# Kernel tuning notes

Hardware: AMD Instinct MI355X
Metric: run time of the kernel (lower is better)

The kernel has to match this reference:

```python
import jax, jax.numpy as jnp
import numpy as np

B, S, D, H, DH = 2, 2048, 1024, 16, 64


def setup_inputs() -> dict:
    key = jax.random.key(0)
    ks = jax.random.split(key, 8)
    std = 0.02
    Q = jax.random.normal(ks[0], (B, S, D), jnp.float32)
    K = jax.random.normal(ks[1], (B, S, D), jnp.float32)
    V = jax.random.normal(ks[2], (B, S, D), jnp.float32)
    # 0/1 float mask, 1 = masked out (causal upper triangle), shape [B, S, S]
    causal = jnp.triu(jnp.ones((S, S), jnp.float32), k=1)
    attn_mask = jnp.broadcast_to(causal, (B, S, S))
    Wq = jax.random.normal(ks[3], (D, H * DH), jnp.float32) * std
    Wk = jax.random.normal(ks[4], (D, H * DH), jnp.float32) * std
    Wv = jax.random.normal(ks[5], (D, H * DH), jnp.float32) * std
    Wo = jax.random.normal(ks[6], (H * DH, D), jnp.float32) * std
    bq = jnp.zeros((H * DH,), jnp.float32)
    bk = jnp.zeros((H * DH,), jnp.float32)
    bv = jnp.zeros((H * DH,), jnp.float32)
    bo = jnp.zeros((D,), jnp.float32)
    return dict(Q=Q, K=K, V=V, attn_mask=attn_mask,
                Wq=Wq, bq=bq, Wk=Wk, bk=bk, Wv=Wv, bv=bv, Wo=Wo, bo=bo)


def reference(Q, K, V, attn_mask, Wq, bq, Wk, bk, Wv, bv, Wo, bo):
    b = Q.shape[0]
    # projections + split heads: [B, S, H*DH] -> [B, H, S, DH]
    def heads(x, W, bias):
        y = x @ W + bias
        return y.reshape(b, -1, H, DH).transpose(0, 2, 1, 3)
    Qh = heads(Q, Wq, bq)
    Kh = heads(K, Wk, bk)
    Vh = heads(V, Wv, bv)
    scale = jnp.sqrt(jnp.asarray(DH, jnp.float32))
    # [B, H, Sq, Sk]
    scores = jnp.einsum('bhqd,bhkd->bhqk', Qh, Kh) / scale
    scores = scores - 1e9 * attn_mask[:, None, :, :]
    probs = jax.nn.softmax(scores, axis=-1)
    out = jnp.einsum('bhqk,bhkd->bhqd', probs, Vh)  # [B, H, Sq, DH]
    out = out.transpose(0, 2, 1, 3).reshape(b, -1, H * DH)
    return out @ Wo + bo
```

## Files before the change

### kernel.cpp

```cpp
#include <hip/hip_runtime.h>
#include <hip/hip_bf16.h>

#define S_LEN 2048
#define NH 16
#define DHD 64

typedef __attribute__((ext_vector_type(8))) short bf16x8;
typedef __attribute__((ext_vector_type(4))) float f32x4;

__device__ __forceinline__ f32x4 mfma16(bf16x8 a, bf16x8 b, f32x4 c) {
  return __builtin_amdgcn_mfma_f32_16x16x32_bf16(a, b, c, 0, 0, 0);
}

union Pack8 { int4 v; __hip_bfloat16 h[8]; };

__device__ __forceinline__ unsigned pack_bf16(float lo, float hi) {
  union { __hip_bfloat16 b; unsigned short s; } a0, a1;
  a0.b = __float2bfloat16(lo);
  a1.b = __float2bfloat16(hi);
  return (unsigned)a0.s | ((unsigned)a1.s << 16);
}

__global__ __launch_bounds__(256) void transpose_cast(
    const float* __restrict__ W0, const float* __restrict__ W1,
    const float* __restrict__ W2, const float* __restrict__ W3,
    __hip_bfloat16* __restrict__ T0, __hip_bfloat16* __restrict__ T1,
    __hip_bfloat16* __restrict__ T2, __hip_bfloat16* __restrict__ T3) {
  __shared__ float t[32][33];
  const float* W;
  __hip_bfloat16* T;
  switch (blockIdx.z) {
    case 0: W = W0; T = T0; break;
    case 1: W = W1; T = T1; break;
    case 2: W = W2; T = T2; break;
    default: W = W3; T = T3; break;
  }
  const int tx = threadIdx.x, ty = threadIdx.y;
  const int c = blockIdx.x * 32 + tx;
  const int r0 = blockIdx.y * 32;
#pragma unroll
  for (int i = ty; i < 32; i += 8) t[i][tx] = W[(r0 + i) * 1024 + c];
  __syncthreads();
  const int c0 = blockIdx.x * 32;
#pragma unroll
  for (int i = ty; i < 32; i += 8)
    T[(c0 + i) * 1024 + (r0 + tx)] = __float2bfloat16(t[tx][i]);
}

#define LDP 72

__global__ __launch_bounds__(256) void qkv_gemm(
    const float* __restrict__ Qx, const float* __restrict__ Kx,
    const float* __restrict__ Vx,
    const __hip_bfloat16* __restrict__ WqT, const __hip_bfloat16* __restrict__ WkT,
    const __hip_bfloat16* __restrict__ WvT,
    const float* __restrict__ bq, const float* __restrict__ bk,
    const float* __restrict__ bv,
    __hip_bfloat16* __restrict__ Qh, __hip_bfloat16* __restrict__ Kh,
    __hip_bfloat16* __restrict__ Vt) {
  __shared__ __hip_bfloat16 sA[128 * LDP];
  __shared__ __hip_bfloat16 sB[128 * LDP];
  const int K = 1024;
  const int yy = blockIdx.y;
  const int sel = yy >> 3;
  const int m0 = blockIdx.x * 128;
  const int n0 = (yy & 7) * 128;
  const float* X = sel == 0 ? Qx : sel == 1 ? Kx : Vx;
  const __hip_bfloat16* Bt = sel == 0 ? WqT : sel == 1 ? WkT : WvT;
  const float* bias = sel == 0 ? bq : sel == 1 ? bk : bv;
  __hip_bfloat16* outp = sel == 0 ? Qh : sel == 1 ? Kh : Vt;
  const float scale = sel == 0 ? 0.18033688011112042f : 1.0f;
  const int tid = threadIdx.x;
  const int lane = tid & 63;
  const int wv = tid >> 6;
  const int wm = (wv >> 1) * 64;
  const int wn = (wv & 1) * 64;
  const int rq = lane & 15;
  const int kg = lane >> 4;
  f32x4 acc[4][4] = {};
  for (int k0 = 0; k0 < K; k0 += 64) {
#pragma unroll
    for (int j = 0; j < 4; ++j) {
      const int cid = j * 256 + tid;
      const int row = cid >> 3;
      const int kc = (cid & 7) * 8;
      const float* ap = X + (m0 + row) * K + k0 + kc;
      float4 f0 = *(const float4*)ap;
      float4 f1 = *(const float4*)(ap + 4);
      Pack8 p;
      p.h[0] = __float2bfloat16(f0.x); p.h[1] = __float2bfloat16(f0.y);
      p.h[2] = __float2bfloat16(f0.z); p.h[3] = __float2bfloat16(f0.w);
      p.h[4] = __float2bfloat16(f1.x); p.h[5] = __float2bfloat16(f1.y);
      p.h[6] = __float2bfloat16(f1.z); p.h[7] = __float2bfloat16(f1.w);
      *(int4*)&sA[row * LDP + kc] = p.v;
      *(int4*)&sB[row * LDP + kc] = *(const int4*)(Bt + (n0 + row) * K + k0 + kc);
    }
    __syncthreads();
#pragma unroll
    for (int kk = 0; kk < 2; ++kk) {
      bf16x8 af[4], bfr[4];
      const int kcol = kk * 32 + kg * 8;
#pragma unroll
      for (int mi = 0; mi < 4; ++mi)
        af[mi] = *(const bf16x8*)&sA[(wm + mi * 16 + rq) * LDP + kcol];
#pragma unroll
      for (int ni = 0; ni < 4; ++ni)
        bfr[ni] = *(const bf16x8*)&sB[(wn + ni * 16 + rq) * LDP + kcol];
#pragma unroll
      for (int mi = 0; mi < 4; ++mi)
#pragma unroll
        for (int ni = 0; ni < 4; ++ni)
          acc[mi][ni] = mfma16(af[mi], bfr[ni], acc[mi][ni]);
    }
    __syncthreads();
  }
  const int cr = (lane >> 4) << 2;
  const int cc = lane & 15;
#pragma unroll
  for (int ni = 0; ni < 4; ++ni) {
    const int col = n0 + wn + ni * 16 + cc;
    const float bv_ = bias[col];
#pragma unroll
    for (int mi = 0; mi < 4; ++mi) {
      const int rowb = m0 + wm + mi * 16 + cr;
#pragma unroll
      for (int r = 0; r < 4; ++r) {
        const int row = rowb + r;
        const float v = (acc[mi][ni][r] + bv_) * scale;
        const int b = row >> 11, s = row & 2047, h = col >> 6, dh = col & 63;
        const __hip_bfloat16 hv = __float2bfloat16(v);
        if (sel < 2)
          outp[((b * NH + h) * S_LEN + s) * DHD + dh] = hv;
        else
          outp[((b * NH + h) * DHD + dh) * S_LEN + s] = hv;
      }
    }
  }
}

__global__ __launch_bounds__(256) void out_gemm(
    const __hip_bfloat16* __restrict__ Aptr, const __hip_bfloat16* __restrict__ Bt,
    const float* __restrict__ bias, float* __restrict__ outp) {
  __shared__ __hip_bfloat16 sA[128 * LDP];
  __shared__ __hip_bfloat16 sB[128 * LDP];
  const int K = 1024;
  const int m0 = blockIdx.x * 128;
  const int n0 = blockIdx.y * 128;
  const int tid = threadIdx.x;
  const int lane = tid & 63;
  const int wv = tid >> 6;
  const int wm = (wv >> 1) * 64;
  const int wn = (wv & 1) * 64;
  const int rq = lane & 15;
  const int kg = lane >> 4;
  f32x4 acc[4][4] = {};
  for (int k0 = 0; k0 < K; k0 += 64) {
#pragma unroll
    for (int j = 0; j < 4; ++j) {
      const int cid = j * 256 + tid;
      const int row = cid >> 3;
      const int kc = (cid & 7) * 8;
      *(int4*)&sA[row * LDP + kc] = *(const int4*)(Aptr + (m0 + row) * K + k0 + kc);
      *(int4*)&sB[row * LDP + kc] = *(const int4*)(Bt + (n0 + row) * K + k0 + kc);
    }
    __syncthreads();
#pragma unroll
    for (int kk = 0; kk < 2; ++kk) {
      bf16x8 af[4], bfr[4];
      const int kcol = kk * 32 + kg * 8;
#pragma unroll
      for (int mi = 0; mi < 4; ++mi)
        af[mi] = *(const bf16x8*)&sA[(wm + mi * 16 + rq) * LDP + kcol];
#pragma unroll
      for (int ni = 0; ni < 4; ++ni)
        bfr[ni] = *(const bf16x8*)&sB[(wn + ni * 16 + rq) * LDP + kcol];
#pragma unroll
      for (int mi = 0; mi < 4; ++mi)
#pragma unroll
        for (int ni = 0; ni < 4; ++ni)
          acc[mi][ni] = mfma16(af[mi], bfr[ni], acc[mi][ni]);
    }
    __syncthreads();
  }
  const int cr = (lane >> 4) << 2;
  const int cc = lane & 15;
#pragma unroll
  for (int ni = 0; ni < 4; ++ni) {
    const int col = n0 + wn + ni * 16 + cc;
    const float bv = bias[col];
#pragma unroll
    for (int mi = 0; mi < 4; ++mi) {
      const int rowb = m0 + wm + mi * 16 + cr;
#pragma unroll
      for (int r = 0; r < 4; ++r)
        outp[(rowb + r) * 1024 + col] = acc[mi][ni][r] + bv;
    }
  }
}

#define SLOT 2304
#define NSLOT 320

__global__ __launch_bounds__(256) void attn_fwd(
    const __hip_bfloat16* __restrict__ Qh, const __hip_bfloat16* __restrict__ Kh,
    const __hip_bfloat16* __restrict__ Vt, __hip_bfloat16* __restrict__ AttO,
    unsigned char* __restrict__ Part) {
  __shared__ __hip_bfloat16 sK[64 * 72];
  __shared__ __hip_bfloat16 sV[64 * 72];
  const int tid = threadIdx.x;
  const int lane = tid & 63;
  const int wv = tid >> 6;
  const int h = blockIdx.y, b = blockIdx.z;
  const int bh = b * NH + h;
  const int u = 79 - (int)blockIdx.x;
  int j, s;
  if (u < 8)       { j = u; s = 0; }
  else if (u < 24) { int v = u - 8;  j = 8 + (v >> 1);  s = v & 1; }
  else if (u < 48) { int v = u - 24; int q3 = v / 3; j = 16 + q3; s = v - 3 * q3; }
  else             { int v = u - 48; j = 24 + (v >> 2); s = v & 3; }
  const int ns = (j >> 3) + 1;
  const int kv_beg = s * 512;
  const int kv_end = min(kv_beg + 512, j * 64 + 64);
  const int nt = (kv_end - kv_beg + 63) >> 6;

  const int i_tile = 4 * j + wv;
  const int q0 = i_tile * 16;
  const int qmax = q0 + 15;
  const __hip_bfloat16* Qb = Qh + bh * (S_LEN * DHD);
  const __hip_bfloat16* Kb = Kh + bh * (S_LEN * DHD);
  const __hip_bfloat16* Vb = Vt + bh * (DHD * S_LEN);
  const int c = lane & 15;
  const int g = lane >> 4;
  const bf16x8 qf0 = *(const bf16x8*)&Qb[(q0 + c) * DHD + g * 8];
  const bf16x8 qf1 = *(const bf16x8*)&Qb[(q0 + c) * DHD + 32 + g * 8];
  f32x4 o[4] = {};
  float m_run = -1e30f, l_run = 0.f;
  const int idx_lo = c + ((lane & 16) << 1);
  const int idx_hi = idx_lo + 16;
  const int lim0 = q0 + c - (g << 2);
  const bool hi_half = (lane & 32) != 0;

  const int srow = tid >> 2;
  const int scol = (tid & 3) << 4;
  int4 ka0, ka1, va0, va1;
#define ISSUE_LOADS(KV0)                                                  \
  ka0 = *(const int4*)&Kb[(KV0 + srow) * DHD + scol];                     \
  ka1 = *(const int4*)&Kb[(KV0 + srow) * DHD + scol + 8];                 \
  va0 = *(const int4*)&Vb[srow * S_LEN + (KV0) + scol];                   \
  va1 = *(const int4*)&Vb[srow * S_LEN + (KV0) + scol + 8];
#define STORE_LDS()                                                       \
  *(int4*)&sK[srow * 72 + scol] = ka0;                                    \
  *(int4*)&sK[srow * 72 + scol + 8] = ka1;                                \
  *(int4*)&sV[srow * 72 + scol] = va0;                                    \
  *(int4*)&sV[srow * 72 + scol + 8] = va1;

  ISSUE_LOADS(kv_beg);
  STORE_LDS();
  __syncthreads();

  for (int t = 0; t < nt; ++t) {
    const int kv0 = kv_beg + t * 64;
    const bool havenext = (t + 1 < nt);
    if (havenext) { ISSUE_LOADS(kv0 + 64); }
    if (kv0 <= qmax) {
      f32x4 sc[4] = {};
#pragma unroll
      for (int fi = 0; fi < 4; ++fi) {
        const bf16x8 ka = *(const bf16x8*)&sK[(fi * 16 + c) * 72 + g * 8];
        const bf16x8 kb = *(const bf16x8*)&sK[(fi * 16 + c) * 72 + 32 + g * 8];
        sc[fi] = mfma16(ka, qf0, sc[fi]);
        sc[fi] = mfma16(kb, qf1, sc[fi]);
      }
      if (kv0 + 63 > q0) {
        const int lim = lim0 - kv0;
#pragma unroll
        for (int fi = 0; fi < 4; ++fi)
#pragma unroll
          for (int r = 0; r < 4; ++r)
            if (fi * 16 + r > lim) sc[fi][r] = -1e30f;
      }
      float pm = fmaxf(fmaxf(fmaxf(sc[0][0], sc[0][1]), fmaxf(sc[0][2], sc[0][3])),
                       fmaxf(fmaxf(sc[1][0], sc[1][1]), fmaxf(sc[1][2], sc[1][3])));
      pm = fmaxf(pm, fmaxf(fmaxf(fmaxf(sc[2][0], sc[2][1]), fmaxf(sc[2][2], sc[2][3])),
                           fmaxf(fmaxf(sc[3][0], sc[3][1]), fmaxf(sc[3][2], sc[3][3]))));
      pm = fmaxf(pm, __shfl_xor(pm, 16));
      pm = fmaxf(pm, __shfl_xor(pm, 32));
      if (__any(pm > m_run + 8.0f)) {
        const float mn = fmaxf(m_run, pm);
        const float al = __builtin_amdgcn_exp2f(m_run - mn);
        m_run = mn;
        l_run *= al;
#pragma unroll
        for (int jj = 0; jj < 4; ++jj)
#pragma unroll
          for (int r = 0; r < 4; ++r) o[jj][r] *= al;
      }
      f32x4 p[4];
      float ps = 0.f;
#pragma unroll
      for (int fi = 0; fi < 4; ++fi) {
#pragma unroll
        for (int r = 0; r < 4; ++r) {
          p[fi][r] = __builtin_amdgcn_exp2f(sc[fi][r] - m_run);
          ps += p[fi][r];
        }
      }
      ps += __shfl_xor(ps, 16);
      ps += __shfl_xor(ps, 32);
      l_run += ps;
      unsigned w0[4], w1[4];
#pragma unroll
      for (int fi = 0; fi < 4; ++fi) {
        w0[fi] = pack_bf16(p[fi][0], p[fi][1]);
        w1[fi] = pack_bf16(p[fi][2], p[fi][3]);
      }
#pragma unroll
      for (int kk = 0; kk < 2; ++kk) {
        const int fA = 2 * kk, fB = 2 * kk + 1;
        union { unsigned w[4]; bf16x8 v; } pa;
        unsigned a0 = __shfl((int)w0[fA], idx_lo), b0 = __shfl((int)w0[fB], idx_lo);
        unsigned a1 = __shfl((int)w1[fA], idx_lo), b1 = __shfl((int)w1[fB], idx_lo);
        unsigned a2 = __shfl((int)w0[fA], idx_hi), b2 = __shfl((int)w0[fB], idx_hi);
        unsigned a3 = __shfl((int)w1[fA], idx_hi), b3 = __shfl((int)w1[fB], idx_hi);
        pa.w[0] = hi_half ? b0 : a0;
        pa.w[1] = hi_half ? b1 : a1;
        pa.w[2] = hi_half ? b2 : a2;
        pa.w[3] = hi_half ? b3 : a3;
#pragma unroll
        for (int jj = 0; jj < 4; ++jj) {
          const bf16x8 vf = *(const bf16x8*)&sV[(jj * 16 + c) * 72 + kk * 32 + g * 8];
          o[jj] = mfma16(vf, pa.v, o[jj]);
        }
      }
    }
    if (havenext) {
      __syncthreads();
      STORE_LDS();
      __syncthreads();
    }
  }

  if (ns == 1) {
    const float inv = 1.0f / l_run;
    __hip_bfloat16* op = AttO + (size_t)(b * S_LEN + q0 + c) * 1024 + h * DHD;
#pragma unroll
    for (int jj = 0; jj < 4; ++jj) {
      unsigned lo = pack_bf16(o[jj][0] * inv, o[jj][1] * inv);
      unsigned hi = pack_bf16(o[jj][2] * inv, o[jj][3] * inv);
      *(uint2*)&op[jj * 16 + (g << 2)] = make_uint2(lo, hi);
    }
  } else {
    int xr;
    if (i_tile < 64) xr = 32 + 2 * (i_tile - 32) + s;
    else if (i_tile < 96) xr = 96 + 3 * (i_tile - 64) + s;
    else xr = 192 + 4 * (i_tile - 96) + s;
    unsigned char* slot = Part + (size_t)(bh * NSLOT + xr) * SLOT;
    __hip_bfloat16* ob = (__hip_bfloat16*)slot;
#pragma unroll
    for (int jj = 0; jj < 4; ++jj) {
      unsigned lo = pack_bf16(o[jj][0], o[jj][1]);
      unsigned hi = pack_bf16(o[jj][2], o[jj][3]);
      *(uint2*)&ob[c * DHD + jj * 16 + (g << 2)] = make_uint2(lo, hi);
    }
    if (lane < 16) {
      *(float*)(slot + 2048 + lane * 4) = m_run;
      *(float*)(slot + 2112 + lane * 4) = l_run;
    }
  }
#undef ISSUE_LOADS
#undef STORE_LDS
}

__global__ __launch_bounds__(64) void attn_combine(
    const unsigned char* __restrict__ Part, __hip_bfloat16* __restrict__ AttO) {
  const int i = 32 + (int)blockIdx.x;
  const int h = blockIdx.y, b = blockIdx.z;
  const int bh = b * NH + h;
  const int ns = (i >> 5) + 1;
  int xr0;
  if (i < 64) xr0 = 32 + 2 * (i - 32);
  else if (i < 96) xr0 = 96 + 3 * (i - 64);
  else xr0 = 192 + 4 * (i - 96);
  const int lane = threadIdx.x;
  const int q = lane >> 2, qa = lane & 3;
  const unsigned char* base = Part + (size_t)(bh * NSLOT + xr0) * SLOT;
  float M = -1e30f;
  for (int s = 0; s < ns; ++s)
    M = fmaxf(M, *(const float*)(base + s * SLOT + 2048 + q * 4));
  float O[16] = {};
  float L = 0.f;
  for (int s = 0; s < ns; ++s) {
    const unsigned char* sp = base + s * SLOT;
    const float ms = *(const float*)(sp + 2048 + q * 4);
    const float ls = *(const float*)(sp + 2112 + q * 4);
    const float scale = __builtin_amdgcn_exp2f(ms - M);
    L += ls * scale;
    Pack8 w0, w1;
    w0.v = *(const int4*)(sp + (q * DHD + qa * 16) * 2);
    w1.v = *(const int4*)(sp + (q * DHD + qa * 16 + 8) * 2);
#pragma unroll
    for (int e = 0; e < 8; ++e) {
      O[e] += __bfloat162float(w0.h[e]) * scale;
      O[8 + e] += __bfloat162float(w1.h[e]) * scale;
    }
  }
  const float inv = 1.0f / L;
  Pack8 r0, r1;
#pragma unroll
  for (int e = 0; e < 8; ++e) {
    r0.h[e] = __float2bfloat16(O[e] * inv);
    r1.h[e] = __float2bfloat16(O[8 + e] * inv);
  }
  __hip_bfloat16* op = AttO + (size_t)(b * S_LEN + i * 16 + q) * 1024 + h * DHD + qa * 16;
  *(int4*)op = r0.v;
  *(int4*)(op + 8) = r1.v;
}

extern "C" void kernel_launch(void* const* d_in, const int* in_sizes, int n_in,
                              void* d_out, int out_size, void* d_ws, size_t ws_size,
                              hipStream_t stream) {
  const float* Qx = (const float*)d_in[0];
  const float* Kx = (const float*)d_in[1];
  const float* Vx = (const float*)d_in[2];
  const float* Wq = (const float*)d_in[4];
  const float* bq = (const float*)d_in[5];
  const float* Wk = (const float*)d_in[6];
  const float* bk = (const float*)d_in[7];
  const float* Wv = (const float*)d_in[8];
  const float* bv = (const float*)d_in[9];
  const float* Wo = (const float*)d_in[10];
  const float* bo = (const float*)d_in[11];

  __hip_bfloat16* ws = (__hip_bfloat16*)d_ws;
  __hip_bfloat16* WqT = ws;
  __hip_bfloat16* WkT = ws + (1u << 20);
  __hip_bfloat16* WvT = ws + (2u << 20);
  __hip_bfloat16* WoT = ws + (3u << 20);
  __hip_bfloat16* Qh  = ws + (4u << 20);
  __hip_bfloat16* Kh  = ws + (8u << 20);
  __hip_bfloat16* Vt  = ws + (12u << 20);
  __hip_bfloat16* AttO = ws + (16u << 20);
  unsigned char* Part = (unsigned char*)(ws + (20u << 20));

  transpose_cast<<<dim3(32, 32, 4), dim3(32, 8), 0, stream>>>(
      Wq, Wk, Wv, Wo, WqT, WkT, WvT, WoT);
  qkv_gemm<<<dim3(32, 24), 256, 0, stream>>>(
      Qx, Kx, Vx, WqT, WkT, WvT, bq, bk, bv, Qh, Kh, Vt);
  attn_fwd<<<dim3(80, 16, 2), 256, 0, stream>>>(Qh, Kh, Vt, AttO, Part);
  attn_combine<<<dim3(96, 16, 2), 64, 0, stream>>>(Part, AttO);
  out_gemm<<<dim3(32, 8), 256, 0, stream>>>(AttO, WoT, bo, (float*)d_out);
}
```

Before: 149.6 us.

## Load GEMM tiles directly to LDS via global_load_lds, cast A in LDS

Replaces register-staged global-to-LDS tile loads in the QKV and output projection GEMMs with direct global_load_lds 16-byte transfers. In qkv_gemm the fp32 activations are now stored in LDS unconverted and cast to bf16 at fragment-read time, which doubles A-tile LDS footprint and moves the conversion into the inner loop. The padded LDS stride is dropped in favour of unpadded 64-wide rows, so fragment reads may see more bank conflicts. The loop is still single-buffered with two barriers per k-step.

Result: slower. 175.5 us (+17.3%).

```diff
diff --git a/kernel.cpp b/kernel.cpp
--- a/kernel.cpp
+++ b/kernel.cpp
@@ -19,6 +19,13 @@
   a0.b = __float2bfloat16(lo);
   a1.b = __float2bfloat16(hi);
   return (unsigned)a0.s | ((unsigned)a1.s << 16);
+}
+
+__device__ __forceinline__ void gload_lds16(const void* g, void* l) {
+  __builtin_amdgcn_global_load_lds(
+      (const __attribute__((address_space(1))) void*)(unsigned long long)g,
+      (__attribute__((address_space(3))) void*)(unsigned long long)l,
+      16, 0, 0);
 }
 
 __global__ __launch_bounds__(256) void transpose_cast(
@@ -47,8 +54,6 @@
     T[(c0 + i) * 1024 + (r0 + tx)] = __float2bfloat16(t[tx][i]);
 }
 
-#define LDP 72
-
 __global__ __launch_bounds__(256) void qkv_gemm(
     const float* __restrict__ Qx, const float* __restrict__ Kx,
     const float* __restrict__ Vx,
@@ -58,8 +63,8 @@
     const float* __restrict__ bv,
     __hip_bfloat16* __restrict__ Qh, __hip_bfloat16* __restrict__ Kh,
     __hip_bfloat16* __restrict__ Vt) {
-  __shared__ __hip_bfloat16 sA[128 * LDP];
-  __shared__ __hip_bfloat16 sB[128 * LDP];
+  __shared__ float sAf[128 * 64];
+  __shared__ __hip_bfloat16 sB[128 * 64];
   const int K = 1024;
   const int yy = blockIdx.y;
   const int sel = yy >> 3;
@@ -77,35 +82,43 @@
   const int wn = (wv & 1) * 64;
   const int rq = lane & 15;
   const int kg = lane >> 4;
+  const int arow = lane >> 4;
+  const int acol = (lane & 15) * 4;
+  const int brow = lane >> 3;
+  const int bcol = (lane & 7) * 8;
   f32x4 acc[4][4] = {};
   for (int k0 = 0; k0 < K; k0 += 64) {
 #pragma unroll
-    for (int j = 0; j < 4; ++j) {
-      const int cid = j * 256 + tid;
-      const int row = cid >> 3;
-      const int kc = (cid & 7) * 8;
-      const float* ap = X + (m0 + row) * K + k0 + kc;
-      float4 f0 = *(const float4*)ap;
-      float4 f1 = *(const float4*)(ap + 4);
-      Pack8 p;
-      p.h[0] = __float2bfloat16(f0.x); p.h[1] = __float2bfloat16(f0.y);
-      p.h[2] = __float2bfloat16(f0.z); p.h[3] = __float2bfloat16(f0.w);
-      p.h[4] = __float2bfloat16(f1.x); p.h[5] = __float2bfloat16(f1.y);
-      p.h[6] = __float2bfloat16(f1.z); p.h[7] = __float2bfloat16(f1.w);
-      *(int4*)&sA[row * LDP + kc] = p.v;
-      *(int4*)&sB[row * LDP + kc] = *(const int4*)(Bt + (n0 + row) * K + k0 + kc);
+    for (int i2 = 0; i2 < 8; ++i2) {
+      const int ci = wv * 8 + i2;
+      gload_lds16(X + (size_t)(m0 + ci * 4 + arow) * K + k0 + acol,
+                  (char*)sAf + ci * 1024);
+    }
+#pragma unroll
+    for (int i2 = 0; i2 < 4; ++i2) {
+      const int ci = wv * 4 + i2;
+      gload_lds16(Bt + (size_t)(n0 + ci * 8 + brow) * K + k0 + bcol,
+                  (char*)sB + ci * 1024);
     }
     __syncthreads();
 #pragma unroll
     for (int kk = 0; kk < 2; ++kk) {
       bf16x8 af[4], bfr[4];
-      const int kcol = kk * 32 + kg * 8;
-#pragma unroll
-      for (int mi = 0; mi < 4; ++mi)
-        af[mi] = *(const bf16x8*)&sA[(wm + mi * 16 + rq) * LDP + kcol];
+#pragma unroll
+      for (int mi = 0; mi < 4; ++mi) {
+        const float* ap = &sAf[(wm + mi * 16 + rq) * 64 + kk * 32 + kg * 8];
+        const f32x4 lo = *(const f32x4*)ap;
+        const f32x4 hi = *(const f32x4*)(ap + 4);
+        union { unsigned w[4]; bf16x8 v; } u;
+        u.w[0] = pack_bf16(lo[0], lo[1]);
+        u.w[1] = pack_bf16(lo[2], lo[3]);
+        u.w[2] = pack_bf16(hi[0], hi[1]);
+        u.w[3] = pack_bf16(hi[2], hi[3]);
+        af[mi] = u.v;
+      }
 #pragma unroll
       for (int ni = 0; ni < 4; ++ni)
-        bfr[ni] = *(const bf16x8*)&sB[(wn + ni * 16 + rq) * LDP + kcol];
+        bfr[ni] = *(const bf16x8*)&sB[(wn + ni * 16 + rq) * 64 + kk * 32 + kg * 8];
 #pragma unroll
       for (int mi = 0; mi < 4; ++mi)
 #pragma unroll
@@ -141,8 +154,8 @@
 __global__ __launch_bounds__(256) void out_gemm(
     const __hip_bfloat16* __restrict__ Aptr, const __hip_bfloat16* __restrict__ Bt,
     const float* __restrict__ bias, float* __restrict__ outp) {
-  __shared__ __hip_bfloat16 sA[128 * LDP];
-  __shared__ __hip_bfloat16 sB[128 * LDP];
+  __shared__ __hip_bfloat16 sA[128 * 64];
+  __shared__ __hip_bfloat16 sB[128 * 64];
   const int K = 1024;
   const int m0 = blockIdx.x * 128;
   const int n0 = blockIdx.y * 128;
@@ -153,15 +166,17 @@
   const int wn = (wv & 1) * 64;
   const int rq = lane & 15;
   const int kg = lane >> 4;
+  const int brow = lane >> 3;
+  const int bcol = (lane & 7) * 8;
   f32x4 acc[4][4] = {};
   for (int k0 = 0; k0 < K; k0 += 64) {
 #pragma unroll
-    for (int j = 0; j < 4; ++j) {
-      const int cid = j * 256 + tid;
-      const int row = cid >> 3;
-      const int kc = (cid & 7) * 8;
-      *(int4*)&sA[row * LDP + kc] = *(const int4*)(Aptr + (m0 + row) * K + k0 + kc);
-      *(int4*)&sB[row * LDP + kc] = *(const int4*)(Bt + (n0 + row) * K + k0 + kc);
+    for (int i2 = 0; i2 < 4; ++i2) {
+      const int ci = wv * 4 + i2;
+      gload_lds16(Aptr + (size_t)(m0 + ci * 8 + brow) * K + k0 + bcol,
+                  (char*)sA + ci * 1024);
+      gload_lds16(Bt + (size_t)(n0 + ci * 8 + brow) * K + k0 + bcol,
+                  (char*)sB + ci * 1024);
     }
     __syncthreads();
 #pragma unroll
@@ -170,10 +185,10 @@
       const int kcol = kk * 32 + kg * 8;
 #pragma unroll
       for (int mi = 0; mi < 4; ++mi)
-        af[mi] = *(const bf16x8*)&sA[(wm + mi * 16 + rq) * LDP + kcol];
+        af[mi] = *(const bf16x8*)&sA[(wm + mi * 16 + rq) * 64 + kcol];
 #pragma unroll
       for (int ni = 0; ni < 4; ++ni)
-        bfr[ni] = *(const bf16x8*)&sB[(wn + ni * 16 + rq) * LDP + kcol];
+        bfr[ni] = *(const bf16x8*)&sB[(wn + ni * 16 + rq) * 64 + kcol];
 #pragma unroll
       for (int mi = 0; mi < 4; ++mi)
 #pragma unroll
```

## Pre-cast activations to bf16 and register-prefetch next K tile in GEMMs

Applied to the files above, without the earlier changes.

Adds a separate kernel that converts the Q/K/V fp32 activations to bf16 once, so the QKV GEMM no longer re-reads fp32 and converts for every N tile. Both the QKV and output GEMMs now load the next K tile into registers while the MFMAs run on the current shared-memory tile, then store it after a barrier. This is meant to hide global load latency and cut redundant fp32 traffic. The cost is an extra kernel launch, an extra bf16 buffer write and read, more registers per thread, and one additional barrier per iteration.

Result: slower. 247.4 us (+65.4%).

```diff
diff --git a/kernel.cpp b/kernel.cpp
--- a/kernel.cpp
+++ b/kernel.cpp
@@ -19,6 +19,23 @@
   a0.b = __float2bfloat16(lo);
   a1.b = __float2bfloat16(hi);
   return (unsigned)a0.s | ((unsigned)a1.s << 16);
+}
+
+__global__ __launch_bounds__(256) void cast3_bf16(
+    const float* __restrict__ Qx, const float* __restrict__ Kx,
+    const float* __restrict__ Vx, __hip_bfloat16* __restrict__ Xb) {
+  const int z = blockIdx.y;
+  const float* X = z == 0 ? Qx : z == 1 ? Kx : Vx;
+  __hip_bfloat16* O = Xb + (size_t)z * 4194304u;
+  const size_t base = ((size_t)blockIdx.x * 256 + threadIdx.x) * 8;
+  const float4 f0 = *(const float4*)&X[base];
+  const float4 f1 = *(const float4*)&X[base + 4];
+  Pack8 p;
+  p.h[0] = __float2bfloat16(f0.x); p.h[1] = __float2bfloat16(f0.y);
+  p.h[2] = __float2bfloat16(f0.z); p.h[3] = __float2bfloat16(f0.w);
+  p.h[4] = __float2bfloat16(f1.x); p.h[5] = __float2bfloat16(f1.y);
+  p.h[6] = __float2bfloat16(f1.z); p.h[7] = __float2bfloat16(f1.w);
+  *(int4*)&O[base] = p.v;
 }
 
 __global__ __launch_bounds__(256) void transpose_cast(
@@ -50,8 +67,7 @@
 #define LDP 72
 
 __global__ __launch_bounds__(256) void qkv_gemm(
-    const float* __restrict__ Qx, const float* __restrict__ Kx,
-    const float* __restrict__ Vx,
+    const __hip_bfloat16* __restrict__ Xb,
     const __hip_bfloat16* __restrict__ WqT, const __hip_bfloat16* __restrict__ WkT,
     const __hip_bfloat16* __restrict__ WvT,
     const float* __restrict__ bq, const float* __restrict__ bk,
@@ -65,7 +81,7 @@
   const int sel = yy >> 3;
   const int m0 = blockIdx.x * 128;
   const int n0 = (yy & 7) * 128;
-  const float* X = sel == 0 ? Qx : sel == 1 ? Kx : Vx;
+  const __hip_bfloat16* A = Xb + (size_t)sel * 4194304u;
   const __hip_bfloat16* Bt = sel == 0 ? WqT : sel == 1 ? WkT : WvT;
   const float* bias = sel == 0 ? bq : sel == 1 ? bk : bv;
   __hip_bfloat16* outp = sel == 0 ? Qh : sel == 1 ? Kh : Vt;
@@ -77,25 +93,26 @@
   const int wn = (wv & 1) * 64;
   const int rq = lane & 15;
   const int kg = lane >> 4;
+  const int srow = tid >> 3;
+  const int skc = (tid & 7) * 8;
+  int4 ar[4], br[4];
+#define QISSUE(K0)                                                        \
+  _Pragma("unroll") for (int j = 0; j < 4; ++j) {                         \
+    ar[j] = *(const int4*)&A[(size_t)(m0 + j * 32 + srow) * K + (K0) + skc]; \
+    br[j] = *(const int4*)&Bt[(size_t)(n0 + j * 32 + srow) * K + (K0) + skc]; \
+  }
+#define QSTORE()                                                          \
+  _Pragma("unroll") for (int j = 0; j < 4; ++j) {                         \
+    *(int4*)&sA[(j * 32 + srow) * LDP + skc] = ar[j];                     \
+    *(int4*)&sB[(j * 32 + srow) * LDP + skc] = br[j];                     \
+  }
   f32x4 acc[4][4] = {};
+  QISSUE(0);
+  QSTORE();
+  __syncthreads();
   for (int k0 = 0; k0 < K; k0 += 64) {
-#pragma unroll
-    for (int j = 0; j < 4; ++j) {
-      const int cid = j * 256 + tid;
-      const int row = cid >> 3;
-      const int kc = (cid & 7) * 8;
-      const float* ap = X + (m0 + row) * K + k0 + kc;
-      float4 f0 = *(const float4*)ap;
-      float4 f1 = *(const float4*)(ap + 4);
-      Pack8 p;
-      p.h[0] = __float2bfloat16(f0.x); p.h[1] = __float2bfloat16(f0.y);
-      p.h[2] = __float2bfloat16(f0.z); p.h[3] = __float2bfloat16(f0.w);
-      p.h[4] = __float2bfloat16(f1.x); p.h[5] = __float2bfloat16(f1.y);
-      p.h[6] = __float2bfloat16(f1.z); p.h[7] = __float2bfloat16(f1.w);
-      *(int4*)&sA[row * LDP + kc] = p.v;
-      *(int4*)&sB[row * LDP + kc] = *(const int4*)(Bt + (n0 + row) * K + k0 + kc);
-    }
-    __syncthreads();
+    const bool havenext = (k0 + 64 < K);
+    if (havenext) { QISSUE(k0 + 64); }
 #pragma unroll
     for (int kk = 0; kk < 2; ++kk) {
       bf16x8 af[4], bfr[4];
@@ -112,8 +129,14 @@
         for (int ni = 0; ni < 4; ++ni)
           acc[mi][ni] = mfma16(af[mi], bfr[ni], acc[mi][ni]);
     }
-    __syncthreads();
-  }
+    if (havenext) {
+      __syncthreads();
+      QSTORE();
+      __syncthreads();
+    }
+  }
+#undef QISSUE
+#undef QSTORE
   const int cr = (lane >> 4) << 2;
   const int cc = lane & 15;
 #pragma unroll
@@ -153,17 +176,26 @@
   const int wn = (wv & 1) * 64;
   const int rq = lane & 15;
   const int kg = lane >> 4;
+  const int srow = tid >> 3;
+  const int skc = (tid & 7) * 8;
+  int4 ar[4], br[4];
+#define OISSUE(K0)                                                        \
+  _Pragma("unroll") for (int j = 0; j < 4; ++j) {                         \
+    ar[j] = *(const int4*)&Aptr[(size_t)(m0 + j * 32 + srow) * K + (K0) + skc]; \
+    br[j] = *(const int4*)&Bt[(size_t)(n0 + j * 32 + srow) * K + (K0) + skc]; \
+  }
+#define OSTORE()                                                          \
+  _Pragma("unroll") for (int j = 0; j < 4; ++j) {                         \
+    *(int4*)&sA[(j * 32 + srow) * LDP + skc] = ar[j];                     \
+    *(int4*)&sB[(j * 32 + srow) * LDP + skc] = br[j];                     \
+  }
   f32x4 acc[4][4] = {};
+  OISSUE(0);
+  OSTORE();
+  __syncthreads();
   for (int k0 = 0; k0 < K; k0 += 64) {
-#pragma unroll
-    for (int j = 0; j < 4; ++j) {
-      const int cid = j * 256 + tid;
-      const int row = cid >> 3;
-      const int kc = (cid & 7) * 8;
-      *(int4*)&sA[row * LDP + kc] = *(const int4*)(Aptr + (m0 + row) * K + k0 + kc);
-      *(int4*)&sB[row * LDP + kc] = *(const int4*)(Bt + (n0 + row) * K + k0 + kc);
-    }
-    __syncthreads();
+    const bool havenext = (k0 + 64 < K);
+    if (havenext) { OISSUE(k0 + 64); }
 #pragma unroll
     for (int kk = 0; kk < 2; ++kk) {
       bf16x8 af[4], bfr[4];
@@ -180,8 +212,14 @@
         for (int ni = 0; ni < 4; ++ni)
           acc[mi][ni] = mfma16(af[mi], bfr[ni], acc[mi][ni]);
     }
-    __syncthreads();
-  }
+    if (havenext) {
+      __syncthreads();
+      OSTORE();
+      __syncthreads();
+    }
+  }
+#undef OISSUE
+#undef OSTORE
   const int cr = (lane >> 4) << 2;
   const int cc = lane & 15;
 #pragma unroll
@@ -441,11 +479,13 @@
   __hip_bfloat16* Vt  = ws + (12u << 20);
   __hip_bfloat16* AttO = ws + (16u << 20);
   unsigned char* Part = (unsigned char*)(ws + (20u << 20));
-
+  __hip_bfloat16* Xb = (__hip_bfloat16*)(Part + (size_t)32 * NSLOT * SLOT);
+
+  cast3_bf16<<<dim3(2048, 3), 256, 0, stream>>>(Qx, Kx, Vx, Xb);
   transpose_cast<<<dim3(32, 32, 4), dim3(32, 8), 0, stream>>>(
       Wq, Wk, Wv, Wo, WqT, WkT, WvT, WoT);
   qkv_gemm<<<dim3(32, 24), 256, 0, stream>>>(
-      Qx, Kx, Vx, WqT, WkT, WvT, bq, bk, bv, Qh, Kh, Vt);
+      Xb, WqT, WkT, WvT, bq, bk, bv, Qh, Kh, Vt);
   attn_fwd<<<dim3(80, 16, 2), 256, 0, stream>>>(Qh, Kh, Vt, AttO, Part);
   attn_combine<<<dim3(96, 16, 2), 64, 0, stream>>>(Part, AttO);
   out_gemm<<<dim3(32, 8), 256, 0, stream>>>(AttO, WoT, bo, (float*)d_out);
```

## Pre-cast QKV inputs to bf16 and use direct global-to-LDS loads in QKV GEMM

Applied to the files above, without the earlier changes.

Adds a separate kernel that casts the Q, K and V fp32 activations to bf16 once into workspace. The QKV GEMM then loads A and B tiles with global_load_lds (direct global-to-LDS DMA) instead of loading fp32 into registers, converting, and storing to LDS. In the old scheme each input row was re-cast by every N-tile block. The LDS padding is dropped to fit the DMA layout, which may cause bank conflicts on the MFMA fragment reads. It also adds an extra launch and a full bf16 write and read of the inputs.

New measurement: 161.6 us. 8.0% more time.

```diff
diff --git a/kernel.cpp b/kernel.cpp
--- a/kernel.cpp
+++ b/kernel.cpp
@@ -19,6 +19,30 @@
   a0.b = __float2bfloat16(lo);
   a1.b = __float2bfloat16(hi);
   return (unsigned)a0.s | ((unsigned)a1.s << 16);
+}
+
+__device__ __forceinline__ void gload_lds16(const void* g, void* l) {
+  __builtin_amdgcn_global_load_lds(
+      (const __attribute__((address_space(1))) void*)(unsigned long long)g,
+      (__attribute__((address_space(3))) void*)(unsigned long long)l,
+      16, 0, 0);
+}
+
+__global__ __launch_bounds__(256) void cast3_bf16(
+    const float* __restrict__ Qx, const float* __restrict__ Kx,
+    const float* __restrict__ Vx, __hip_bfloat16* __restrict__ Xb) {
+  const int z = blockIdx.y;
+  const float* X = z == 0 ? Qx : z == 1 ? Kx : Vx;
+  __hip_bfloat16* O = Xb + (size_t)z * 4194304u;
+  const size_t base = ((size_t)blockIdx.x * 256 + threadIdx.x) * 8;
+  const float4 f0 = *(const float4*)&X[base];
+  const float4 f1 = *(const float4*)&X[base + 4];
+  Pack8 p;
+  p.h[0] = __float2bfloat16(f0.x); p.h[1] = __float2bfloat16(f0.y);
+  p.h[2] = __float2bfloat16(f0.z); p.h[3] = __float2bfloat16(f0.w);
+  p.h[4] = __float2bfloat16(f1.x); p.h[5] = __float2bfloat16(f1.y);
+  p.h[6] = __float2bfloat16(f1.z); p.h[7] = __float2bfloat16(f1.w);
+  *(int4*)&O[base] = p.v;
 }
 
 __global__ __launch_bounds__(256) void transpose_cast(
@@ -47,25 +71,22 @@
     T[(c0 + i) * 1024 + (r0 + tx)] = __float2bfloat16(t[tx][i]);
 }
 
-#define LDP 72
-
 __global__ __launch_bounds__(256) void qkv_gemm(
-    const float* __restrict__ Qx, const float* __restrict__ Kx,
-    const float* __restrict__ Vx,
+    const __hip_bfloat16* __restrict__ Xb,
     const __hip_bfloat16* __restrict__ WqT, const __hip_bfloat16* __restrict__ WkT,
     const __hip_bfloat16* __restrict__ WvT,
     const float* __restrict__ bq, const float* __restrict__ bk,
     const float* __restrict__ bv,
     __hip_bfloat16* __restrict__ Qh, __hip_bfloat16* __restrict__ Kh,
     __hip_bfloat16* __restrict__ Vt) {
-  __shared__ __hip_bfloat16 sA[128 * LDP];
-  __shared__ __hip_bfloat16 sB[128 * LDP];
+  __shared__ __hip_bfloat16 sA[128 * 64];
+  __shared__ __hip_bfloat16 sB[128 * 64];
   const int K = 1024;
   const int yy = blockIdx.y;
   const int sel = yy >> 3;
   const int m0 = blockIdx.x * 128;
   const int n0 = (yy & 7) * 128;
-  const float* X = sel == 0 ? Qx : sel == 1 ? Kx : Vx;
+  const __hip_bfloat16* A = Xb + (size_t)sel * 4194304u;
   const __hip_bfloat16* Bt = sel == 0 ? WqT : sel == 1 ? WkT : WvT;
   const float* bias = sel == 0 ? bq : sel == 1 ? bk : bv;
   __hip_bfloat16* outp = sel == 0 ? Qh : sel == 1 ? Kh : Vt;
@@ -77,23 +98,17 @@
   const int wn = (wv & 1) * 64;
   const int rq = lane & 15;
   const int kg = lane >> 4;
+  const int brow = lane >> 3;
+  const int bcol = (lane & 7) * 8;
   f32x4 acc[4][4] = {};
   for (int k0 = 0; k0 < K; k0 += 64) {
 #pragma unroll
-    for (int j = 0; j < 4; ++j) {
-      const int cid = j * 256 + tid;
-      const int row = cid >> 3;
-      const int kc = (cid & 7) * 8;
-      const float* ap = X + (m0 + row) * K + k0 + kc;
-      float4 f0 = *(const float4*)ap;
-      float4 f1 = *(const float4*)(ap + 4);
-      Pack8 p;
-      p.h[0] = __float2bfloat16(f0.x); p.h[1] = __float2bfloat16(f0.y);
-      p.h[2] = __float2bfloat16(f0.z); p.h[3] = __float2bfloat16(f0.w);
-      p.h[4] = __float2bfloat16(f1.x); p.h[5] = __float2bfloat16(f1.y);
-      p.h[6] = __float2bfloat16(f1.z); p.h[7] = __float2bfloat16(f1.w);
-      *(int4*)&sA[row * LDP + kc] = p.v;
-      *(int4*)&sB[row * LDP + kc] = *(const int4*)(Bt + (n0 + row) * K + k0 + kc);
+    for (int i2 = 0; i2 < 4; ++i2) {
+      const int ci = wv * 4 + i2;
+      gload_lds16(A + (size_t)(m0 + ci * 8 + brow) * K + k0 + bcol,
+                  (char*)sA + ci * 1024);
+      gload_lds16(Bt + (size_t)(n0 + ci * 8 + brow) * K + k0 + bcol,
+                  (char*)sB + ci * 1024);
     }
     __syncthreads();
 #pragma unroll
@@ -102,10 +117,10 @@
       const int kcol = kk * 32 + kg * 8;
 #pragma unroll
       for (int mi = 0; mi < 4; ++mi)
-        af[mi] = *(const bf16x8*)&sA[(wm + mi * 16 + rq) * LDP + kcol];
+        af[mi] = *(const bf16x8*)&sA[(wm + mi * 16 + rq) * 64 + kcol];
 #pragma unroll
       for (int ni = 0; ni < 4; ++ni)
-        bfr[ni] = *(const bf16x8*)&sB[(wn + ni * 16 + rq) * LDP + kcol];
+        bfr[ni] = *(const bf16x8*)&sB[(wn + ni * 16 + rq) * 64 + kcol];
 #pragma unroll
       for (int mi = 0; mi < 4; ++mi)
 #pragma unroll
@@ -137,6 +152,8 @@
     }
   }
 }
+
+#define LDP 72
 
 __global__ __launch_bounds__(256) void out_gemm(
     const __hip_bfloat16* __restrict__ Aptr, const __hip_bfloat16* __restrict__ Bt,
@@ -441,11 +458,13 @@
   __hip_bfloat16* Vt  = ws + (12u << 20);
   __hip_bfloat16* AttO = ws + (16u << 20);
   unsigned char* Part = (unsigned char*)(ws + (20u << 20));
-
+  __hip_bfloat16* Xb = (__hip_bfloat16*)(Part + (size_t)32 * NSLOT * SLOT);
+
+  cast3_bf16<<<dim3(2048, 3), 256, 0, stream>>>(Qx, Kx, Vx, Xb);
   transpose_cast<<<dim3(32, 32, 4), dim3(32, 8), 0, stream>>>(
       Wq, Wk, Wv, Wo, WqT, WkT, WvT, WoT);
   qkv_gemm<<<dim3(32, 24), 256, 0, stream>>>(
-      Qx, Kx, Vx, WqT, WkT, WvT, bq, bk, bv, Qh, Kh, Vt);
+      Xb, WqT, WkT, WvT, bq, bk, bv, Qh, Kh, Vt);
   attn_fwd<<<dim3(80, 16, 2), 256, 0, stream>>>(Qh, Kh, Vt, AttO, Part);
   attn_combine<<<dim3(96, 16, 2), 64, 0, stream>>>(Part, AttO);
   out_gemm<<<dim3(32, 8), 256, 0, stream>>>(AttO, WoT, bo, (float*)d_out);
```
